# Optimization experiments

Measured on AMD Instinct MI355X. Metric: run time of the kernel, lower is better.

The kernel has to match this reference:

```python
import jax, jax.numpy as jnp
import numpy as np

N_EMBD = 1024
N_HEADS = 16
HEAD_SIZE = N_EMBD // N_HEADS  # 64
B, T = 4, 4096


def setup_inputs() -> dict:
    key = jax.random.key(0)
    kx, kq, kk, kv = jax.random.split(key, 4)
    scale = 1.0 / np.sqrt(N_EMBD)
    x = jax.random.normal(kx, (B, T, N_EMBD), dtype=jnp.float32)
    # torch Linear weight shape: (out_features, in_features)
    Wq = jax.random.normal(kq, (HEAD_SIZE, N_EMBD), dtype=jnp.float32) * scale
    Wk = jax.random.normal(kk, (HEAD_SIZE, N_EMBD), dtype=jnp.float32) * scale
    Wv = jax.random.normal(kv, (HEAD_SIZE, N_EMBD), dtype=jnp.float32) * scale
    return {"x": x, "Wq": Wq, "Wk": Wk, "Wv": Wv}


def reference(x, Wq, Wk, Wv):
    # q,k,v: [B, T, H]  (H = head_size)
    q = jnp.einsum('btc,hc->bth', x, Wq)
    k = jnp.einsum('btc,hc->bth', x, Wk)
    v = jnp.einsum('btc,hc->bth', x, Wv)
    # scores: [B, T, T], scaled by head_size**-0.5
    wei = jnp.einsum('bth,bsh->bts', q, k) * (HEAD_SIZE ** -0.5)
    Tlen = x.shape[1]
    causal = jnp.tril(jnp.ones((Tlen, Tlen), dtype=bool))
    wei = jnp.where(causal, wei, -jnp.inf)
    wei = jax.nn.softmax(wei, axis=-1)
    # dropout p=0.0 (eval) -> identity
    out = jnp.einsum('bts,bsh->bth', wei, v)  # [B, T, H]
    return out
```

## Files before the change

kernel.cpp:

```cpp
#include <hip/hip_runtime.h>
#include <math.h>

#define B_ 4
#define T_ 4096
#define C_ 1024
#define H_ 64
#define NROW (B_ * T_)

typedef unsigned short u16;
typedef __attribute__((ext_vector_type(8))) short short8;
typedef __attribute__((ext_vector_type(4))) float floatx4;
typedef __attribute__((ext_vector_type(8))) unsigned short ushortx8;
typedef __attribute__((ext_vector_type(4))) unsigned short ushortx4;

__device__ __forceinline__ u16 f2bf(float f) {
  unsigned int u = __builtin_bit_cast(unsigned int, f);
  unsigned int r = (u + 0x7FFFu + ((u >> 16) & 1u)) >> 16;
  return (u16)r;
}

__global__ __launch_bounds__(256) void cast_w_kernel(
    const float* __restrict__ Wq, const float* __restrict__ Wk,
    const float* __restrict__ Wv, u16* __restrict__ Wb) {
  int i = blockIdx.x * 256 + threadIdx.x;
  const float* src = (i < 16384) ? Wq : ((i < 32768) ? Wk : Wv);
  int j = i & 16383;
  float4 v = ((const float4*)src)[j];
  ushortx4 o = {f2bf(v.x), f2bf(v.y), f2bf(v.z), f2bf(v.w)};
  *(ushortx4*)(Wb + (size_t)i * 4) = o;
}

__global__ __launch_bounds__(256) void proj9_kernel(
    const float* __restrict__ x, const u16* __restrict__ Wb,
    u16* __restrict__ Qb, u16* __restrict__ Kb, u16* __restrict__ Vt) {
  const int m0 = (int)blockIdx.x * 64;
  const int tid = threadIdx.x;
  const int wave = tid >> 6, lane = tid & 63;
  const int lq = lane & 15, quad = lane >> 4;

  __shared__ __align__(16) u16 xs[64 * 1024];

  const u16* wp0 = Wb + (size_t)((wave * 3 + 0) * 16 + lq) * C_ + quad * 8;
  const u16* wp1 = Wb + (size_t)((wave * 3 + 1) * 16 + lq) * C_ + quad * 8;
  const u16* wp2 = Wb + (size_t)((wave * 3 + 2) * 16 + lq) * C_ + quad * 8;
  short8 wf[4][3];
#pragma unroll
  for (int d = 0; d < 4; ++d) {
    wf[d][0] = *(const short8*)(wp0 + d * 32);
    wf[d][1] = *(const short8*)(wp1 + d * 32);
    wf[d][2] = *(const short8*)(wp2 + d * 32);
  }

#pragma unroll 4
  for (int i = 0; i < 32; ++i) {
    int g = i * 256 + tid;
    int row = g >> 7, c = g & 127;
    const float* src = x + (size_t)(m0 + row) * C_ + c * 8;
    float4 a = *(const float4*)(src);
    float4 b = *(const float4*)(src + 4);
    ushortx8 v = {f2bf(a.x), f2bf(a.y), f2bf(a.z), f2bf(a.w),
                  f2bf(b.x), f2bf(b.y), f2bf(b.z), f2bf(b.w)};
    *(ushortx8*)&xs[(row * 128 + (c ^ (row & 7))) * 8] = v;
  }
  __syncthreads();

  floatx4 acc[4][3];
#pragma unroll
  for (int rt = 0; rt < 4; ++rt)
#pragma unroll
    for (int j = 0; j < 3; ++j) acc[rt][j] = (floatx4){0.f, 0.f, 0.f, 0.f};

#pragma unroll
  for (int s = 0; s < 32; ++s) {
    short8 af[4];
#pragma unroll
    for (int rt = 0; rt < 4; ++rt) {
      int row = rt * 16 + lq;
      int c = (s * 4 + quad) ^ (lq & 7);
      af[rt] = *(const short8*)&xs[(row * 128 + c) * 8];
    }
    const int sl = s & 3;
#pragma unroll
    for (int j = 0; j < 3; ++j) {
      short8 bf = wf[sl][j];
#pragma unroll
      for (int rt = 0; rt < 4; ++rt)
        acc[rt][j] =
            __builtin_amdgcn_mfma_f32_16x16x32_bf16(af[rt], bf, acc[rt][j], 0, 0, 0);
    }
    if (s + 4 < 32) {
      wf[sl][0] = *(const short8*)(wp0 + (s + 4) * 32);
      wf[sl][1] = *(const short8*)(wp1 + (s + 4) * 32);
      wf[sl][2] = *(const short8*)(wp2 + (s + 4) * 32);
    }
  }

  __syncthreads();
  u16(*sm)[208] = (u16(*)[208])xs;
#pragma unroll
  for (int j = 0; j < 3; ++j) {
    const int gc = (wave * 3 + j) * 16;
    const float sc = (gc < 64) ? 0.18033688011112042f : 1.0f;
#pragma unroll
    for (int rt = 0; rt < 4; ++rt)
#pragma unroll
      for (int r = 0; r < 4; ++r)
        sm[rt * 16 + quad * 4 + r][gc + lq] = f2bf(acc[rt][j][r] * sc);
  }
  __syncthreads();

  const int row = tid >> 2, hseg = (tid & 3) * 16;
  {
    ushortx8 w0 = *(const ushortx8*)&sm[row][hseg];
    ushortx8 w1 = *(const ushortx8*)&sm[row][hseg + 8];
    u16* dq = Qb + (size_t)(m0 + row) * H_ + hseg;
    *(ushortx8*)dq = w0;
    *(ushortx8*)(dq + 8) = w1;
  }
  {
    ushortx8 w0 = *(const ushortx8*)&sm[row][64 + hseg];
    ushortx8 w1 = *(const ushortx8*)&sm[row][64 + hseg + 8];
    u16* dk = Kb + (size_t)(m0 + row) * H_ + hseg;
    *(ushortx8*)dk = w0;
    *(ushortx8*)(dk + 8) = w1;
  }
  {
    const int h = tid >> 2, tseg = (tid & 3) * 16;
    u16 tmp[16];
#pragma unroll
    for (int tt = 0; tt < 16; ++tt) tmp[tt] = sm[tseg + tt][128 + h];
    ushortx8 w0, w1;
#pragma unroll
    for (int tt = 0; tt < 8; ++tt) { w0[tt] = tmp[tt]; w1[tt] = tmp[8 + tt]; }
    const int bb = m0 >> 12, t0 = m0 & 4095;
    u16* dv = Vt + ((size_t)bb * H_ + h) * T_ + t0 + tseg;
    *(ushortx8*)dv = w0;
    *(ushortx8*)(dv + 8) = w1;
  }
}

__global__ __launch_bounds__(256, 4) void attn_kernel(
    const u16* __restrict__ Qb, const u16* __restrict__ Kb,
    const u16* __restrict__ Vt, float* __restrict__ Opart,
    float* __restrict__ lpart, int KS, int kslog) {
  const int tau = (int)gridDim.x - 1 - (int)blockIdx.x;
  const int q0 = tau * 128;
  const int b = (int)blockIdx.y >> kslog;
  const int s = (int)blockIdx.y & (KS - 1);
  const int tid = threadIdx.x;
  const int wave = tid >> 6, lane = tid & 63;
  const int lq = lane & 15, quad = lane >> 4;

  __shared__ __align__(16) u16 ps[4][32 * 72];

  const int nchw = 2 * tau + 1 + (wave >> 1);
  const u16* Kb_b = Kb + (size_t)b * T_ * H_;
  const u16* Vt_b = Vt + (size_t)b * H_ * T_;

  short8 qa[2][2];
#pragma unroll
  for (int rt = 0; rt < 2; ++rt) {
    const u16* qrow =
        Qb + ((size_t)b * T_ + q0 + wave * 32 + rt * 16 + lq) * H_;
    qa[rt][0] = *(const short8*)(qrow + quad * 8);
    qa[rt][1] = *(const short8*)(qrow + 32 + quad * 8);
  }

  floatx4 o[2][4];
  float lrow[2] = {0.f, 0.f};
#pragma unroll
  for (int rt = 0; rt < 2; ++rt)
#pragma unroll
    for (int t = 0; t < 4; ++t) o[rt][t] = (floatx4){0.f, 0.f, 0.f, 0.f};

  const float nbias = -5.770780163555852f;

  for (int ch = s; ch < nchw; ch += KS) {
    const int s0 = ch * 64;

    floatx4 z[2][4];
#pragma unroll
    for (int t = 0; t < 4; ++t) {
      const u16* krow = Kb_b + (size_t)(s0 + t * 16 + lq) * H_;
      short8 kb0 = *(const short8*)(krow + quad * 8);
      short8 kb1 = *(const short8*)(krow + 32 + quad * 8);
#pragma unroll
      for (int rt = 0; rt < 2; ++rt) {
        floatx4 zz = (floatx4){nbias, nbias, nbias, nbias};
        zz = __builtin_amdgcn_mfma_f32_16x16x32_bf16(kb0, qa[rt][0], zz, 0, 0, 0);
        zz = __builtin_amdgcn_mfma_f32_16x16x32_bf16(kb1, qa[rt][1], zz, 0, 0, 0);
        z[rt][t] = zz;
      }
    }

#pragma unroll
    for (int rt = 0; rt < 2; ++rt) {
      const int qr = q0 + wave * 32 + rt * 16 + lq;
      const bool nm = (s0 + 63 > q0 + wave * 32 + rt * 16);
#pragma unroll
      for (int t = 0; t < 4; ++t) {
        float p0 = exp2f(z[rt][t][0]);
        float p1 = exp2f(z[rt][t][1]);
        float p2 = exp2f(z[rt][t][2]);
        float p3 = exp2f(z[rt][t][3]);
        if (nm) {
          const int k0 = s0 + t * 16 + quad * 4;
          p0 = (k0 + 0 > qr) ? 0.f : p0;
          p1 = (k0 + 1 > qr) ? 0.f : p1;
          p2 = (k0 + 2 > qr) ? 0.f : p2;
          p3 = (k0 + 3 > qr) ? 0.f : p3;
        }
        lrow[rt] += (p0 + p1) + (p2 + p3);
        ushortx4 pk = {f2bf(p0), f2bf(p1), f2bf(p2), f2bf(p3)};
        *(ushortx4*)&ps[wave][(rt * 16 + lq) * 72 + t * 16 + quad * 4] = pk;
      }
    }

    short8 pa[2][2];
#pragma unroll
    for (int rt = 0; rt < 2; ++rt) {
      pa[rt][0] = *(const short8*)&ps[wave][(rt * 16 + lq) * 72 + quad * 8];
      pa[rt][1] =
          *(const short8*)&ps[wave][(rt * 16 + lq) * 72 + 32 + quad * 8];
    }

#pragma unroll
    for (int t = 0; t < 4; ++t) {
      const u16* vrow = Vt_b + (size_t)(t * 16 + lq) * T_ + s0;
      short8 vb0 = *(const short8*)(vrow + quad * 8);
      short8 vb1 = *(const short8*)(vrow + 32 + quad * 8);
#pragma unroll
      for (int rt = 0; rt < 2; ++rt) {
        o[rt][t] = __builtin_amdgcn_mfma_f32_16x16x32_bf16(pa[rt][0], vb0,
                                                           o[rt][t], 0, 0, 0);
        o[rt][t] = __builtin_amdgcn_mfma_f32_16x16x32_bf16(pa[rt][1], vb1,
                                                           o[rt][t], 0, 0, 0);
      }
    }
  }

#pragma unroll
  for (int rt = 0; rt < 2; ++rt) {
    lrow[rt] += __shfl_xor(lrow[rt], 16);
    lrow[rt] += __shfl_xor(lrow[rt], 32);
  }

  const size_t prow = (size_t)((b << kslog) + s) * T_ + q0 + wave * 32;
#pragma unroll
  for (int rt = 0; rt < 2; ++rt) {
#pragma unroll
    for (int t = 0; t < 4; ++t)
#pragma unroll
      for (int r = 0; r < 4; ++r)
        Opart[(prow + rt * 16 + quad * 4 + r) * H_ + t * 16 + lq] =
            o[rt][t][r];
    if (quad == 0) lpart[prow + rt * 16 + lq] = lrow[rt];
  }
}

__global__ __launch_bounds__(256) void combine_kernel(
    const float* __restrict__ Opart, const float* __restrict__ lpart,
    float* __restrict__ out, int KS, int kslog) {
  int gid = blockIdx.x * 256 + threadIdx.x;
  int b = gid >> 16;
  int rem = gid & 65535;
  int t = rem >> 4;
  int hs = (rem & 15) * 4;
  float sx = 0.f, sy = 0.f, sz = 0.f, sw = 0.f, ls = 0.f;
  for (int s = 0; s < KS; ++s) {
    size_t row = (size_t)((b << kslog) + s) * T_ + t;
    float4 v = *(const float4*)(Opart + row * H_ + hs);
    sx += v.x; sy += v.y; sz += v.z; sw += v.w;
    ls += lpart[row];
  }
  float inv = 1.f / ls;
  float4 o = make_float4(sx * inv, sy * inv, sz * inv, sw * inv);
  *(float4*)(out + ((size_t)b * T_ + t) * H_ + hs) = o;
}

extern "C" void kernel_launch(void* const* d_in, const int* in_sizes, int n_in,
                              void* d_out, int out_size, void* d_ws, size_t ws_size,
                              hipStream_t stream) {
  const float* x = (const float*)d_in[0];
  const float* Wq = (const float*)d_in[1];
  const float* Wk = (const float*)d_in[2];
  const float* Wv = (const float*)d_in[3];
  u16* Qb = (u16*)d_ws;
  u16* Kb = Qb + (size_t)NROW * H_;
  u16* Vt = Kb + (size_t)NROW * H_;
  u16* Wb = Vt + (size_t)NROW * H_;
  const size_t base = (size_t)3 * NROW * H_ * 2 + 192 * 1024 * 2;

  int KS = 8;
  while (KS > 1 &&
         base + (size_t)KS * ((size_t)B_ * T_ * H_ * 4 + (size_t)B_ * T_ * 4) >
             ws_size)
    KS >>= 1;
  int kslog = (KS == 8) ? 3 : (KS == 4) ? 2 : (KS == 2) ? 1 : 0;

  float* Opart = (float*)((char*)d_ws + base);
  float* lpart = Opart + (size_t)KS * B_ * T_ * H_;
  float* out = (float*)d_out;

  cast_w_kernel<<<dim3(192), 256, 0, stream>>>(Wq, Wk, Wv, Wb);
  proj9_kernel<<<dim3(256), 256, 0, stream>>>(x, Wb, Qb, Kb, Vt);
  attn_kernel<<<dim3(32, B_ * KS), 256, 0, stream>>>(Qb, Kb, Vt, Opart, lpart,
                                                     KS, kslog);
  combine_kernel<<<dim3(1024), 256, 0, stream>>>(Opart, lpart, out, KS, kslog);
}
```

Measured before the change: 179.9 us.

## Stage K and V tiles in shared memory with double buffering

Instead of each wave loading K and V fragments directly from global memory, the block cooperatively loads each 64-key chunk of K and V^T into XOR-swizzled shared memory. It double-buffers with a register prefetch of the next chunk while the current one is computed. Waves skip chunks fully above their causal range, and the launch-bounds occupancy hint is dropped. This cuts redundant global/L2 traffic across the four waves, at the cost of extra LDS use (32KB more), block-wide barriers, and possibly lower occupancy.

```diff
diff --git a/kernel.cpp b/kernel.cpp
--- a/kernel.cpp
+++ b/kernel.cpp
@@ -139,7 +139,7 @@
   }
 }
 
-__global__ __launch_bounds__(256, 4) void attn_kernel(
+__global__ __launch_bounds__(256) void attn_kernel(
     const u16* __restrict__ Qb, const u16* __restrict__ Kb,
     const u16* __restrict__ Vt, float* __restrict__ Opart,
     float* __restrict__ lpart, int KS, int kslog) {
@@ -150,10 +150,13 @@
   const int tid = threadIdx.x;
   const int wave = tid >> 6, lane = tid & 63;
   const int lq = lane & 15, quad = lane >> 4;
-
+  const int sw = lq & 7;
+
+  __shared__ __align__(16) u16 ksh[2][64 * 64];
+  __shared__ __align__(16) u16 vsh[2][64 * 64];
   __shared__ __align__(16) u16 ps[4][32 * 72];
 
-  const int nchw = 2 * tau + 1 + (wave >> 1);
+  const int nch = 2 * tau + 2;
   const u16* Kb_b = Kb + (size_t)b * T_ * H_;
   const u16* Vt_b = Vt + (size_t)b * H_ * T_;
 
@@ -175,67 +178,108 @@
 
   const float nbias = -5.770780163555852f;
 
-  for (int ch = s; ch < nchw; ch += KS) {
-    const int s0 = ch * 64;
-
-    floatx4 z[2][4];
-#pragma unroll
-    for (int t = 0; t < 4; ++t) {
-      const u16* krow = Kb_b + (size_t)(s0 + t * 16 + lq) * H_;
-      short8 kb0 = *(const short8*)(krow + quad * 8);
-      short8 kb1 = *(const short8*)(krow + 32 + quad * 8);
-#pragma unroll
-      for (int rt = 0; rt < 2; ++rt) {
-        floatx4 zz = (floatx4){nbias, nbias, nbias, nbias};
-        zz = __builtin_amdgcn_mfma_f32_16x16x32_bf16(kb0, qa[rt][0], zz, 0, 0, 0);
-        zz = __builtin_amdgcn_mfma_f32_16x16x32_bf16(kb1, qa[rt][1], zz, 0, 0, 0);
-        z[rt][t] = zz;
+  const int srow = tid >> 3;
+  const int sseg = tid & 7;
+  const int spos0 = (srow * 8 + (sseg ^ (srow & 7))) * 8;
+  const int spos1 = spos0 + 2048;
+
+  int4 kst0, kst1, vst0, vst1;
+#define STAGE_LOAD(S0)                                                        \
+  {                                                                           \
+    kst0 = *(const int4*)(Kb_b + (size_t)((S0) + srow) * H_ + sseg * 8);      \
+    kst1 = *(const int4*)(Kb_b + (size_t)((S0) + srow + 32) * H_ + sseg * 8); \
+    vst0 = *(const int4*)(Vt_b + (size_t)srow * T_ + (S0) + sseg * 8);        \
+    vst1 = *(const int4*)(Vt_b + (size_t)(srow + 32) * T_ + (S0) + sseg * 8); \
+  }
+#define STAGE_WRITE(BUF)                                                      \
+  {                                                                           \
+    *(int4*)&ksh[BUF][spos0] = kst0;                                          \
+    *(int4*)&ksh[BUF][spos1] = kst1;                                          \
+    *(int4*)&vsh[BUF][spos0] = vst0;                                          \
+    *(int4*)&vsh[BUF][spos1] = vst1;                                          \
+  }
+
+  int ch = s, buf = 0;
+  if (ch < nch) {
+    STAGE_LOAD(ch * 64)
+    STAGE_WRITE(0)
+  }
+  __syncthreads();
+
+  if (ch < nch) {
+    const int qmaxw = q0 + wave * 32 + 31;
+    for (;;) {
+      const bool have_next = (ch + KS < nch);
+      if (have_next) { STAGE_LOAD((ch + KS) * 64) }
+      const int s0 = ch * 64;
+
+      if (s0 <= qmaxw) {
+        floatx4 z[2][4];
+#pragma unroll
+        for (int t = 0; t < 4; ++t) {
+          const int row8 = (t * 16 + lq) * 8;
+          short8 kb0 = *(const short8*)&ksh[buf][(row8 + (quad ^ sw)) * 8];
+          short8 kb1 = *(const short8*)&ksh[buf][(row8 + ((quad + 4) ^ sw)) * 8];
+#pragma unroll
+          for (int rt = 0; rt < 2; ++rt) {
+            floatx4 zz = (floatx4){nbias, nbias, nbias, nbias};
+            zz = __builtin_amdgcn_mfma_f32_16x16x32_bf16(kb0, qa[rt][0], zz, 0, 0, 0);
+            zz = __builtin_amdgcn_mfma_f32_16x16x32_bf16(kb1, qa[rt][1], zz, 0, 0, 0);
+            z[rt][t] = zz;
+          }
+        }
+
+#pragma unroll
+        for (int rt = 0; rt < 2; ++rt) {
+          const int qr = q0 + wave * 32 + rt * 16 + lq;
+          const bool nm = (s0 + 63 > q0 + wave * 32 + rt * 16);
+#pragma unroll
+          for (int t = 0; t < 4; ++t) {
+            float p0 = exp2f(z[rt][t][0]);
+            float p1 = exp2f(z[rt][t][1]);
+            float p2 = exp2f(z[rt][t][2]);
+            float p3 = exp2f(z[rt][t][3]);
+            if (nm) {
+              const int k0 = s0 + t * 16 + quad * 4;
+              p0 = (k0 + 0 > qr) ? 0.f : p0;
+              p1 = (k0 + 1 > qr) ? 0.f : p1;
+              p2 = (k0 + 2 > qr) ? 0.f : p2;
+              p3 = (k0 + 3 > qr) ? 0.f : p3;
+            }
+            lrow[rt] += (p0 + p1) + (p2 + p3);
+            ushortx4 pk = {f2bf(p0), f2bf(p1), f2bf(p2), f2bf(p3)};
+            *(ushortx4*)&ps[wave][(rt * 16 + lq) * 72 + t * 16 + quad * 4] = pk;
+          }
+        }
+
+        short8 pa[2][2];
+#pragma unroll
+        for (int rt = 0; rt < 2; ++rt) {
+          pa[rt][0] = *(const short8*)&ps[wave][(rt * 16 + lq) * 72 + quad * 8];
+          pa[rt][1] =
+              *(const short8*)&ps[wave][(rt * 16 + lq) * 72 + 32 + quad * 8];
+        }
+
+#pragma unroll
+        for (int t = 0; t < 4; ++t) {
+          const int row8 = (t * 16 + lq) * 8;
+          short8 vb0 = *(const short8*)&vsh[buf][(row8 + (quad ^ sw)) * 8];
+          short8 vb1 = *(const short8*)&vsh[buf][(row8 + ((quad + 4) ^ sw)) * 8];
+#pragma unroll
+          for (int rt = 0; rt < 2; ++rt) {
+            o[rt][t] = __builtin_amdgcn_mfma_f32_16x16x32_bf16(pa[rt][0], vb0,
+                                                               o[rt][t], 0, 0, 0);
+            o[rt][t] = __builtin_amdgcn_mfma_f32_16x16x32_bf16(pa[rt][1], vb1,
+                                                               o[rt][t], 0, 0, 0);
+          }
+        }
       }
-    }
-
-#pragma unroll
-    for (int rt = 0; rt < 2; ++rt) {
-      const int qr = q0 + wave * 32 + rt * 16 + lq;
-      const bool nm = (s0 + 63 > q0 + wave * 32 + rt * 16);
-#pragma unroll
-      for (int t = 0; t < 4; ++t) {
-        float p0 = exp2f(z[rt][t][0]);
-        float p1 = exp2f(z[rt][t][1]);
-        float p2 = exp2f(z[rt][t][2]);
-        float p3 = exp2f(z[rt][t][3]);
-        if (nm) {
-          const int k0 = s0 + t * 16 + quad * 4;
-          p0 = (k0 + 0 > qr) ? 0.f : p0;
-          p1 = (k0 + 1 > qr) ? 0.f : p1;
-          p2 = (k0 + 2 > qr) ? 0.f : p2;
-          p3 = (k0 + 3 > qr) ? 0.f : p3;
-        }
-        lrow[rt] += (p0 + p1) + (p2 + p3);
-        ushortx4 pk = {f2bf(p0), f2bf(p1), f2bf(p2), f2bf(p3)};
-        *(ushortx4*)&ps[wave][(rt * 16 + lq) * 72 + t * 16 + quad * 4] = pk;
-      }
-    }
-
-    short8 pa[2][2];
-#pragma unroll
-    for (int rt = 0; rt < 2; ++rt) {
-      pa[rt][0] = *(const short8*)&ps[wave][(rt * 16 + lq) * 72 + quad * 8];
-      pa[rt][1] =
-          *(const short8*)&ps[wave][(rt * 16 + lq) * 72 + 32 + quad * 8];
-    }
-
-#pragma unroll
-    for (int t = 0; t < 4; ++t) {
-      const u16* vrow = Vt_b + (size_t)(t * 16 + lq) * T_ + s0;
-      short8 vb0 = *(const short8*)(vrow + quad * 8);
-      short8 vb1 = *(const short8*)(vrow + 32 + quad * 8);
-#pragma unroll
-      for (int rt = 0; rt < 2; ++rt) {
-        o[rt][t] = __builtin_amdgcn_mfma_f32_16x16x32_bf16(pa[rt][0], vb0,
-                                                           o[rt][t], 0, 0, 0);
-        o[rt][t] = __builtin_amdgcn_mfma_f32_16x16x32_bf16(pa[rt][1], vb1,
-                                                           o[rt][t], 0, 0, 0);
-      }
+
+      if (!have_next) break;
+      STAGE_WRITE(buf ^ 1)
+      __syncthreads();
+      buf ^= 1;
+      ch += KS;
     }
   }
 
```

Result: faster. 162.6 us (-9.6%).
